# Optimization experiments

Measured on AMD Instinct MI355X. Metric: run time of the kernel, lower is better.

The kernel has to match this reference:

```python
import jax, jax.numpy as jnp
import numpy as np

MIN_RATIO, MAX_RATIO = 0.7, 1.3
MIN_BIAS, MAX_BIAS = -4.0, 4.0
SOFTMAX_SCALE = 3.0


def setup_inputs() -> dict:
    key = jax.random.key(0)
    k1, k2, k3 = jax.random.split(key, 3)
    B, L_org, N = 32, 2048, 21
    org_tensor = jax.random.normal(k1, (B, L_org, N), dtype=jnp.float32)
    # small perturbations so the clamps are active but not saturated
    ratio_minus_one = 0.1 * jax.random.normal(k2, (N,), dtype=jnp.float32)
    bias = 0.5 * jax.random.normal(k3, (N,), dtype=jnp.float32)
    return {"org_tensor": org_tensor, "ratio_minus_one": ratio_minus_one,
            "bias": bias, "to_length": 2048}


def reference(org_tensor, ratio_minus_one, bias, to_length):
    # input_transformation with is_mark=False
    B, L_org, N = org_tensor.shape
    L_to = to_length
    dt = org_tensor.dtype
    # relu-based clamping in the original == clip
    ratio = jnp.clip(ratio_minus_one + 1.0, MIN_RATIO, MAX_RATIO)  # [N]
    b = jnp.clip(bias, MIN_BIAS, MAX_BIAS)                         # [N]
    org_pos = jnp.arange(-L_org, 0, dtype=dt)                      # [L_org]
    # transformed positions are batch-independent: [L_org, N, 1]
    tpos = org_pos[:, None, None] * ratio[None, :, None] + b[None, :, None]
    tgt = jnp.arange(-L_to, 0, dtype=dt)                           # [L_to]
    deltas = (tpos - tgt[None, None, :]) ** 2                      # [L_org, N, L_to]
    weights = jax.nn.softmax(-deltas * SOFTMAX_SCALE, axis=0)      # softmax over L_org
    # einsum 'bont,bon->btn' with batch-independent weights
    out = jnp.einsum('ont,bon->btn', weights, org_tensor)          # [B, L_to, N]
    return out
```

## Files before the change

kernel.cpp:

```cpp
#include <hip/hip_runtime.h>
#include <hip/hip_bf16.h>


constexpr int LORG  = 2048;
constexpr int LTO   = 2048;
constexpr int NCH   = 21;
constexpr int BATCH = 32;
constexpr int W     = 8;
constexpr int NW    = 2 * W + 1;
constexpr int TT    = 64;
constexpr int BH    = 16;
constexpr int XSTR  = 113;
constexpr int NBLK  = NCH * (LTO / TT) * (BATCH / BH);

constexpr float MIN_RATIO = 0.7f, MAX_RATIO = 1.3f;
constexpr float MIN_BIAS  = -4.0f, MAX_BIAS = 4.0f;
constexpr float NEG3LOG2E = -3.0f * 1.4426950408889634f;

__device__ __forceinline__ int compute_o0(float tg, float bb, float ir) {
    const float ocf = (float)LORG + (tg - bb) * ir;
    int o0 = (int)floorf(ocf + 0.5f) - W;
    return max(0, min(LORG - NW, o0));
}

__global__ __launch_bounds__(256) void li_fused(
    const float* __restrict__ x,
    const float* __restrict__ rmo,
    const float* __restrict__ bias,
    float* __restrict__ out)
{
    const int h  = blockIdx.x;
    const int wk = (h & 7) * (NBLK / 8) + (h >> 3);
    const int bh = wk & 1;
    const int tn = wk >> 1;
    const int tt = tn / NCH;
    const int n  = tn - tt * NCH;
    const int t0 = tt * TT;

    const int tid = threadIdx.x;
    const int tl  = tid & 63;
    const int wv  = tid >> 6;
    const int b0  = bh * BH;

    __shared__ float xs[BH][XSTR];

    const float r  = fminf(fmaxf(rmo[n] + 1.0f, MIN_RATIO), MAX_RATIO);
    const float bb = fminf(fmaxf(bias[n], MIN_BIAS), MAX_BIAS);
    const float ir = 1.0f / r;

    const int lo  = compute_o0((float)(t0 - LTO), bb, ir);
    const int hi  = compute_o0((float)(t0 + TT - 1 - LTO), bb, ir);
    const int len = hi + NW - lo;

    const float tg = (float)(t0 + tl - LTO);
    const int   o0 = compute_o0(tg, bb, ir);
    const int base = o0 - lo;
    float d = (float)(o0 - LORG) * r + bb - tg;
    float js = floorf(-d * ir + 0.5f);
    js = fminf(fmaxf(js, 0.0f), 16.0f);
    const float dstar = d + js * r;
    const float m = NEG3LOG2E * dstar * dstar;
    float w[NW];
    float s = 0.0f;
    #pragma unroll
    for (int j = 0; j < NW; ++j) {
        const float e = NEG3LOG2E * d * d - m;
        w[j] = exp2f(e);
        s += w[j];
        d += r;
    }
    const float inv = 1.0f / s;

    for (int bl = wv; bl < BH; bl += 4) {
        const float* col = x + ((size_t)((b0 + bl) * LORG + lo)) * NCH + n;
        for (int i = tl; i < len; i += 64)
            xs[bl][i] = col[(size_t)i * NCH];
    }
    __syncthreads();

    for (int bl = wv; bl < BH; bl += 4) {
        float acc = 0.0f;
        #pragma unroll
        for (int j = 0; j < NW; ++j)
            acc = fmaf(w[j], xs[bl][base + j], acc);
        out[((size_t)(b0 + bl) * LTO + t0 + tl) * NCH + n] = acc * inv;
    }
}

extern "C" void kernel_launch(void* const* d_in, const int* in_sizes, int n_in,
                              void* d_out, int out_size, void* d_ws, size_t ws_size,
                              hipStream_t stream) {
    const float* x    = (const float*)d_in[0];
    const float* rmo  = (const float*)d_in[1];
    const float* bias = (const float*)d_in[2];
    float* out = (float*)d_out;

    li_fused<<<NBLK, 256, 0, stream>>>(x, rmo, bias, out);
}
```

Before: 17.67 us.

## Issue global loads before weight computation and use per-wave LDS without block barrier

All eight global loads per thread are moved ahead of the softmax weight computation so their latency overlaps the exp2 work. Each wave now stages only its own batch rows in a private LDS slice, so the block-wide __syncthreads is removed and waves proceed independently. This assumes len is at most 128 and relies on the lanes of a wave running in lockstep for the LDS write-then-read with no explicit barrier. That dependence on implicit wave synchrony is a correctness risk.

After: 16.93 us. 4.2% less time.

```diff
diff --git a/kernel.cpp b/kernel.cpp
--- a/kernel.cpp
+++ b/kernel.cpp
@@ -10,7 +10,6 @@
 constexpr int NW    = 2 * W + 1;
 constexpr int TT    = 64;
 constexpr int BH    = 16;
-constexpr int XSTR  = 113;
 constexpr int NBLK  = NCH * (LTO / TT) * (BATCH / BH);
 
 constexpr float MIN_RATIO = 0.7f, MAX_RATIO = 1.3f;
@@ -42,7 +41,7 @@
     const int wv  = tid >> 6;
     const int b0  = bh * BH;
 
-    __shared__ float xs[BH][XSTR];
+    __shared__ float xs[4][4][128];
 
     const float r  = fminf(fmaxf(rmo[n] + 1.0f, MIN_RATIO), MAX_RATIO);
     const float bb = fminf(fmaxf(bias[n], MIN_BIAS), MAX_BIAS);
@@ -51,6 +50,19 @@
     const int lo  = compute_o0((float)(t0 - LTO), bb, ir);
     const int hi  = compute_o0((float)(t0 + TT - 1 - LTO), bb, ir);
     const int len = hi + NW - lo;
+
+    const int i0 = min(tl,      len - 1);
+    const int i1 = min(tl + 64, len - 1);
+
+    const int bA = b0 + wv;
+    const float* colA = x + ((size_t)((bA    ) * LORG + lo)) * NCH + n;
+    const float* colB = x + ((size_t)((bA + 4) * LORG + lo)) * NCH + n;
+    const float* colC = x + ((size_t)((bA + 8) * LORG + lo)) * NCH + n;
+    const float* colD = x + ((size_t)((bA +12) * LORG + lo)) * NCH + n;
+    const float a0 = colA[(size_t)i0 * NCH], a1 = colA[(size_t)i1 * NCH];
+    const float e0 = colB[(size_t)i0 * NCH], e1 = colB[(size_t)i1 * NCH];
+    const float c0 = colC[(size_t)i0 * NCH], c1 = colC[(size_t)i1 * NCH];
+    const float d0 = colD[(size_t)i0 * NCH], d1 = colD[(size_t)i1 * NCH];
 
     const float tg = (float)(t0 + tl - LTO);
     const int   o0 = compute_o0(tg, bb, ir);
@@ -71,20 +83,31 @@
     }
     const float inv = 1.0f / s;
 
-    for (int bl = wv; bl < BH; bl += 4) {
-        const float* col = x + ((size_t)((b0 + bl) * LORG + lo)) * NCH + n;
-        for (int i = tl; i < len; i += 64)
-            xs[bl][i] = col[(size_t)i * NCH];
-    }
-    __syncthreads();
+    float acc;
 
-    for (int bl = wv; bl < BH; bl += 4) {
-        float acc = 0.0f;
-        #pragma unroll
-        for (int j = 0; j < NW; ++j)
-            acc = fmaf(w[j], xs[bl][base + j], acc);
-        out[((size_t)(b0 + bl) * LTO + t0 + tl) * NCH + n] = acc * inv;
-    }
+    xs[wv][0][tl] = a0; xs[wv][0][tl + 64] = a1;
+    acc = 0.0f;
+    #pragma unroll
+    for (int j = 0; j < NW; ++j) acc = fmaf(w[j], xs[wv][0][base + j], acc);
+    out[((size_t)(bA) * LTO + t0 + tl) * NCH + n] = acc * inv;
+
+    xs[wv][1][tl] = e0; xs[wv][1][tl + 64] = e1;
+    acc = 0.0f;
+    #pragma unroll
+    for (int j = 0; j < NW; ++j) acc = fmaf(w[j], xs[wv][1][base + j], acc);
+    out[((size_t)(bA + 4) * LTO + t0 + tl) * NCH + n] = acc * inv;
+
+    xs[wv][2][tl] = c0; xs[wv][2][tl + 64] = c1;
+    acc = 0.0f;
+    #pragma unroll
+    for (int j = 0; j < NW; ++j) acc = fmaf(w[j], xs[wv][2][base + j], acc);
+    out[((size_t)(bA + 8) * LTO + t0 + tl) * NCH + n] = acc * inv;
+
+    xs[wv][3][tl] = d0; xs[wv][3][tl + 64] = d1;
+    acc = 0.0f;
+    #pragma unroll
+    for (int j = 0; j < NW; ++j) acc = fmaf(w[j], xs[wv][3][base + j], acc);
+    out[((size_t)(bA + 12) * LTO + t0 + tl) * NCH + n] = acc * inv;
 }
 
 extern "C" void kernel_launch(void* const* d_in, const int* in_sizes, int n_in,
```

## Process all channels per block and stage output in shared memory for coalesced stores

Applied to the files above, without the earlier changes.

Each block now handles one (batch, time-tile) pair across all 21 channels, instead of one channel across 16 batches. Output is first staged in shared memory, then written back with contiguous stores, which replaces the stride-21 scatter. Channels are ordered by their window start so the strided input reads overlap better in cache. The cost is that softmax weights are recomputed for every batch instead of being shared across 16 batches, and the code assumes each channel's window fits in 128 entries.

Measured after the change: 17.65 us. About the same (-0.1%).

```diff
diff --git a/kernel.cpp b/kernel.cpp
--- a/kernel.cpp
+++ b/kernel.cpp
@@ -9,9 +9,7 @@
 constexpr int W     = 8;
 constexpr int NW    = 2 * W + 1;
 constexpr int TT    = 64;
-constexpr int BH    = 16;
-constexpr int XSTR  = 113;
-constexpr int NBLK  = NCH * (LTO / TT) * (BATCH / BH);
+constexpr int NBLK  = BATCH * (LTO / TT);
 
 constexpr float MIN_RATIO = 0.7f, MAX_RATIO = 1.3f;
 constexpr float MIN_BIAS  = -4.0f, MAX_BIAS = 4.0f;
@@ -31,60 +29,79 @@
 {
     const int h  = blockIdx.x;
     const int wk = (h & 7) * (NBLK / 8) + (h >> 3);
-    const int bh = wk & 1;
-    const int tn = wk >> 1;
-    const int tt = tn / NCH;
-    const int n  = tn - tt * NCH;
+    const int b  = wk >> 5;
+    const int tt = wk & 31;
     const int t0 = tt * TT;
 
     const int tid = threadIdx.x;
     const int tl  = tid & 63;
     const int wv  = tid >> 6;
-    const int b0  = bh * BH;
 
-    __shared__ float xs[BH][XSTR];
+    __shared__ float xs[NCH][128];
+    __shared__ float osh[TT * NCH];
+    __shared__ float rsh[NCH], bsh[NCH], irsh[NCH];
+    __shared__ int   lov[NCH], lenv[NCH], order[NCH];
 
-    const float r  = fminf(fmaxf(rmo[n] + 1.0f, MIN_RATIO), MAX_RATIO);
-    const float bb = fminf(fmaxf(bias[n], MIN_BIAS), MAX_BIAS);
-    const float ir = 1.0f / r;
-
-    const int lo  = compute_o0((float)(t0 - LTO), bb, ir);
-    const int hi  = compute_o0((float)(t0 + TT - 1 - LTO), bb, ir);
-    const int len = hi + NW - lo;
-
-    const float tg = (float)(t0 + tl - LTO);
-    const int   o0 = compute_o0(tg, bb, ir);
-    const int base = o0 - lo;
-    float d = (float)(o0 - LORG) * r + bb - tg;
-    float js = floorf(-d * ir + 0.5f);
-    js = fminf(fmaxf(js, 0.0f), 16.0f);
-    const float dstar = d + js * r;
-    const float m = NEG3LOG2E * dstar * dstar;
-    float w[NW];
-    float s = 0.0f;
-    #pragma unroll
-    for (int j = 0; j < NW; ++j) {
-        const float e = NEG3LOG2E * d * d - m;
-        w[j] = exp2f(e);
-        s += w[j];
-        d += r;
+    if (tid < NCH) {
+        const float r  = fminf(fmaxf(rmo[tid] + 1.0f, MIN_RATIO), MAX_RATIO);
+        const float bb = fminf(fmaxf(bias[tid], MIN_BIAS), MAX_BIAS);
+        const float ir = 1.0f / r;
+        const int lo = compute_o0((float)(t0 - LTO), bb, ir);
+        const int hi = compute_o0((float)(t0 + TT - 1 - LTO), bb, ir);
+        rsh[tid]  = r;  bsh[tid] = bb;  irsh[tid] = ir;
+        lov[tid]  = lo;
+        lenv[tid] = hi + NW - lo;
     }
-    const float inv = 1.0f / s;
-
-    for (int bl = wv; bl < BH; bl += 4) {
-        const float* col = x + ((size_t)((b0 + bl) * LORG + lo)) * NCH + n;
-        for (int i = tl; i < len; i += 64)
-            xs[bl][i] = col[(size_t)i * NCH];
+    __syncthreads();
+    if (tid < NCH) {
+        const int lo = lov[tid];
+        int rank = 0;
+        for (int mth = 0; mth < NCH; ++mth) {
+            const int lm = lov[mth];
+            rank += (lm < lo) || (lm == lo && mth < tid);
+        }
+        order[rank] = tid;
     }
     __syncthreads();
 
-    for (int bl = wv; bl < BH; bl += 4) {
-        float acc = 0.0f;
+    for (int s = wv; s < NCH; s += 4) {
+        const int n   = order[s];
+        const int lo  = lov[n];
+        const int len = lenv[n];
+        const float* col = x + ((size_t)(b * LORG + lo)) * NCH + n;
+        const int i0 = min(tl,      len - 1);
+        const int i1 = min(tl + 64, len - 1);
+        xs[n][tl]      = col[(size_t)i0 * NCH];
+        xs[n][tl + 64] = col[(size_t)i1 * NCH];
+    }
+
+    const float tg = (float)(t0 + tl - LTO);
+    for (int s = wv; s < NCH; s += 4) {
+        const int n  = order[s];
+        const float r  = rsh[n];
+        const float bb = bsh[n];
+        const float ir = irsh[n];
+        const int   o0 = compute_o0(tg, bb, ir);
+        const int base = o0 - lov[n];
+        float d = (float)(o0 - LORG) * r + bb - tg;
+        float js = floorf(-d * ir + 0.5f);
+        js = fminf(fmaxf(js, 0.0f), 16.0f);
+        const float dstar = d + js * r;
+        const float m = NEG3LOG2E * dstar * dstar;
+        float sum = 0.0f, acc = 0.0f;
         #pragma unroll
-        for (int j = 0; j < NW; ++j)
-            acc = fmaf(w[j], xs[bl][base + j], acc);
-        out[((size_t)(b0 + bl) * LTO + t0 + tl) * NCH + n] = acc * inv;
+        for (int j = 0; j < NW; ++j) {
+            const float wgt = exp2f(NEG3LOG2E * d * d - m);
+            sum += wgt;
+            acc = fmaf(wgt, xs[n][base + j], acc);
+            d += r;
+        }
+        osh[tl * NCH + n] = acc * (1.0f / sum);
     }
+    __syncthreads();
+
+    float* dst = out + ((size_t)b * LTO + t0) * NCH;
+    for (int i = tid; i < TT * NCH; i += 256) dst[i] = osh[i];
 }
 
 extern "C" void kernel_launch(void* const* d_in, const int* in_sizes, int n_in,
```

## Narrow softmax window, widen time tile, give each wave private batch rows

Applied to the files above, without the earlier changes.

The truncated softmax window shrinks from 17 to 9 taps, and the time tile grows to 128 with 8 batches per block. Each wave now loads and consumes only its own two batch rows in shared memory, so the block-wide barrier is gone. Each lane handles two target positions and two batches, which reuses the computed weights across batches. The narrower window cuts exp and FMA work but drops more tail weight, which may hurt accuracy when the ratio is small.

Result: faster. 17.27 us (-2.3%).

```diff
diff --git a/kernel.cpp b/kernel.cpp
--- a/kernel.cpp
+++ b/kernel.cpp
@@ -6,12 +6,12 @@
 constexpr int LTO   = 2048;
 constexpr int NCH   = 21;
 constexpr int BATCH = 32;
-constexpr int W     = 8;
+constexpr int W     = 4;
 constexpr int NW    = 2 * W + 1;
-constexpr int TT    = 64;
-constexpr int BH    = 16;
-constexpr int XSTR  = 113;
-constexpr int NBLK  = NCH * (LTO / TT) * (BATCH / BH);
+constexpr int TT    = 128;
+constexpr int BH    = 8;
+constexpr int XCAP  = 200;
+constexpr int NBLK  = (LTO / TT) * NCH * (BATCH / BH);
 
 constexpr float MIN_RATIO = 0.7f, MAX_RATIO = 1.3f;
 constexpr float MIN_BIAS  = -4.0f, MAX_BIAS = 4.0f;
@@ -29,20 +29,20 @@
     const float* __restrict__ bias,
     float* __restrict__ out)
 {
-    const int h  = blockIdx.x;
-    const int wk = (h & 7) * (NBLK / 8) + (h >> 3);
-    const int bh = wk & 1;
-    const int tn = wk >> 1;
-    const int tt = tn / NCH;
-    const int n  = tn - tt * NCH;
-    const int t0 = tt * TT;
+    const int h    = blockIdx.x;
+    const int wk   = (h & 7) * (NBLK / 8) + (h >> 3);
+    const int bg   = wk & 3;
+    const int rest = wk >> 2;
+    const int n    = rest % NCH;
+    const int tt   = rest / NCH;
+    const int t0   = tt * TT;
+    const int b0   = bg * BH;
 
-    const int tid = threadIdx.x;
-    const int tl  = tid & 63;
-    const int wv  = tid >> 6;
-    const int b0  = bh * BH;
+    const int tid  = threadIdx.x;
+    const int lane = tid & 63;
+    const int wv   = tid >> 6;
 
-    __shared__ float xs[BH][XSTR];
+    __shared__ float xs[BH][XCAP];
 
     const float r  = fminf(fmaxf(rmo[n] + 1.0f, MIN_RATIO), MAX_RATIO);
     const float bb = fminf(fmaxf(bias[n], MIN_BIAS), MAX_BIAS);
@@ -52,38 +52,45 @@
     const int hi  = compute_o0((float)(t0 + TT - 1 - LTO), bb, ir);
     const int len = hi + NW - lo;
 
-    const float tg = (float)(t0 + tl - LTO);
-    const int   o0 = compute_o0(tg, bb, ir);
-    const int base = o0 - lo;
-    float d = (float)(o0 - LORG) * r + bb - tg;
-    float js = floorf(-d * ir + 0.5f);
-    js = fminf(fmaxf(js, 0.0f), 16.0f);
-    const float dstar = d + js * r;
-    const float m = NEG3LOG2E * dstar * dstar;
-    float w[NW];
-    float s = 0.0f;
+    const int mb = wv * 2;
+    {
+        const float* colA = x + ((size_t)((b0 + mb    ) * LORG + lo)) * NCH + n;
+        const float* colB = x + ((size_t)((b0 + mb + 1) * LORG + lo)) * NCH + n;
+        for (int i = lane; i < len; i += 64) {
+            xs[mb    ][i] = colA[(size_t)i * NCH];
+            xs[mb + 1][i] = colB[(size_t)i * NCH];
+        }
+    }
+
     #pragma unroll
-    for (int j = 0; j < NW; ++j) {
-        const float e = NEG3LOG2E * d * d - m;
-        w[j] = exp2f(e);
-        s += w[j];
-        d += r;
-    }
-    const float inv = 1.0f / s;
+    for (int half = 0; half < 2; ++half) {
+        const int   tl = lane + 64 * half;
+        const float tg = (float)(t0 + tl - LTO);
+        const int   o0 = compute_o0(tg, bb, ir);
+        const int base = o0 - lo;
+        float d = (float)(o0 - LORG) * r + bb - tg;
+        float js = floorf(-d * ir + 0.5f);
+        js = fminf(fmaxf(js, 0.0f), 8.0f);
+        const float ds = d + js * r;
+        const float m  = NEG3LOG2E * ds * ds;
+        float w[NW];
+        float sum = 0.0f;
+        #pragma unroll
+        for (int j = 0; j < NW; ++j) {
+            w[j] = exp2f(NEG3LOG2E * d * d - m);
+            sum += w[j];
+            d += r;
+        }
+        const float inv = 1.0f / sum;
 
-    for (int bl = wv; bl < BH; bl += 4) {
-        const float* col = x + ((size_t)((b0 + bl) * LORG + lo)) * NCH + n;
-        for (int i = tl; i < len; i += 64)
-            xs[bl][i] = col[(size_t)i * NCH];
-    }
-    __syncthreads();
-
-    for (int bl = wv; bl < BH; bl += 4) {
-        float acc = 0.0f;
+        float accA = 0.0f, accB = 0.0f;
         #pragma unroll
-        for (int j = 0; j < NW; ++j)
-            acc = fmaf(w[j], xs[bl][base + j], acc);
-        out[((size_t)(b0 + bl) * LTO + t0 + tl) * NCH + n] = acc * inv;
+        for (int j = 0; j < NW; ++j) {
+            accA = fmaf(w[j], xs[mb    ][base + j], accA);
+            accB = fmaf(w[j], xs[mb + 1][base + j], accB);
+        }
+        out[((size_t)(b0 + mb    ) * LTO + t0 + tl) * NCH + n] = accA * inv;
+        out[((size_t)(b0 + mb + 1) * LTO + t0 + tl) * NCH + n] = accB * inv;
     }
 }
 
```
